# Optimization experiments

Measured on AMD Instinct MI355X. Metric: run time of the kernel, lower is better.

Reference implementation:

```python
import jax, jax.numpy as jnp
import numpy as np

D_P, D_T, D_F = 128, 256, 384
D = D_P + D_T + D_F            # 768
NUM_PART, NUM_TIMES, NUM_F0 = 64, 601, 360
NHEAD, NLAYERS, DFF = 12, 6, 2048
CTX, PRED = 1024, 64
BATCH = 8
NEG = -1e9


def sin_emb(vals, d, L, base=10000.0):
    # vectorized version of the per-scalar sin_embedding loop
    i = jnp.arange(d // 2, dtype=jnp.float32)
    wk = base ** (-i / d) * (d / L)
    ang = vals[..., None].astype(jnp.float32) * wk           # [..., d/2]
    return jnp.stack([jnp.sin(ang), jnp.cos(ang)], axis=-1).reshape(vals.shape + (d,))


def layernorm(x, g, b, eps=1e-5):
    mu = jnp.mean(x, axis=-1, keepdims=True)
    var = jnp.var(x, axis=-1, keepdims=True)
    return (x - mu) * jax.lax.rsqrt(var + eps) * g + b


def setup_inputs() -> dict:
    key = jax.random.key(0)
    ks = jax.random.split(key, 20)
    inp = {}
    inp['context_participant'] = jax.random.randint(ks[0], (BATCH, CTX), 0, NUM_PART)
    inp['context_time'] = jax.random.uniform(ks[1], (BATCH, CTX), jnp.float32) * 60.0
    inp['context_f0'] = jax.random.randint(ks[2], (BATCH, CTX), 0, NUM_F0)
    # learned / frozen tables
    inp['part_table'] = jax.random.normal(ks[3], (NUM_PART, D_P), jnp.float32)
    inp['time_table'] = sin_emb(jnp.arange(NUM_TIMES, dtype=jnp.float32), D_T, NUM_TIMES)
    inp['f0_table'] = sin_emb(jnp.arange(NUM_F0, dtype=jnp.float32), D_F, NUM_F0)
    inp['pad'] = jax.random.normal(ks[4], (D,), jnp.float32)
    s = 0.02
    inp['Wqkv'] = jax.random.normal(ks[5], (NLAYERS, 3 * D, D), jnp.float32) * s
    inp['bqkv'] = jnp.zeros((NLAYERS, 3 * D), jnp.float32)
    inp['Wo'] = jax.random.normal(ks[6], (NLAYERS, D, D), jnp.float32) * s
    inp['bo'] = jnp.zeros((NLAYERS, D), jnp.float32)
    inp['ln1_g'] = jnp.ones((NLAYERS, D), jnp.float32)
    inp['ln1_b'] = jnp.zeros((NLAYERS, D), jnp.float32)
    inp['W1'] = jax.random.normal(ks[7], (NLAYERS, DFF, D), jnp.float32) * s
    inp['b1'] = jnp.zeros((NLAYERS, DFF), jnp.float32)
    inp['W2'] = jax.random.normal(ks[8], (NLAYERS, D, DFF), jnp.float32) * s
    inp['b2'] = jnp.zeros((NLAYERS, D), jnp.float32)
    inp['ln2_g'] = jnp.ones((NLAYERS, D), jnp.float32)
    inp['ln2_b'] = jnp.zeros((NLAYERS, D), jnp.float32)
    return inp


def reference(context_participant, context_time, context_f0, part_table, time_table,
              f0_table, pad, Wqkv, bqkv, Wo, bo, ln1_g, ln1_b, W1, b1, W2, b2,
              ln2_g, ln2_b):
    B = context_participant.shape[0]
    emb = jnp.concatenate([
        part_table[context_participant],
        sin_emb(context_time, D_T, NUM_TIMES),
        f0_table[context_f0],
    ], axis=-1)                                               # [B, CTX, D]
    dummy = jnp.broadcast_to(pad[None, None, :], (B, PRED, D))
    x = jnp.concatenate([emb, dummy], axis=1)                 # [B, S, D]
    S = CTX + PRED
    # causal mask with -1e9 above diagonal; target block fully masked (incl. diag)
    mask = jnp.where(jnp.triu(jnp.ones((S, S), bool), k=1), NEG, 0.0).astype(jnp.float32)
    mask = mask.at[CTX:, CTX:].set(NEG)
    hd = D // NHEAD
    scale = 1.0 / jnp.sqrt(jnp.float32(hd))
    for l in range(NLAYERS):
        qkv = x @ Wqkv[l].T + bqkv[l]
        q, k, v = jnp.split(qkv, 3, axis=-1)
        q = q.reshape(B, S, NHEAD, hd)
        k = k.reshape(B, S, NHEAD, hd)
        v = v.reshape(B, S, NHEAD, hd)
        scores = jnp.einsum('bqhd,bkhd->bhqk', q, k) * scale + mask
        attn = jax.nn.softmax(scores, axis=-1)
        ctx = jnp.einsum('bhqk,bkhd->bqhd', attn, v).reshape(B, S, D)
        x = layernorm(x + (ctx @ Wo[l].T + bo[l]), ln1_g[l], ln1_b[l])
        ff = jax.nn.relu(x @ W1[l].T + b1[l]) @ W2[l].T + b2[l]
        x = layernorm(x + ff, ln2_g[l], ln2_b[l])
    pred = x[:, CTX:, :]
    pred_cat_logits = pred[:, :, :D_P] @ part_table.T
    pred_time_logits = pred[:, :, D_P:D_P + D_T] @ time_table.T
    pred_f0_logits = pred[:, :, D_P + D_T:] @ f0_table.T
    return (pred_cat_logits, pred_time_logits, pred_f0_logits)
```

## Files before the change

kernel.cpp:

```cpp
#include <hip/hip_runtime.h>
#include <hip/hip_bf16.h>
#include <math.h>

#define D_P 128
#define D_T 256
#define D_F 384
#define DIM 768
#define NUM_TIMES 601
#define NUM_F0 360
#define NHEAD 12
#define HD 64
#define NLAYERS 6
#define DFF 2048
#define CTX 1024
#define SEQ 1088
#define BATCH 8
#define ROWS (BATCH*SEQ)
#define TDIM3 (3*DIM)
#define PREDROWS 512

typedef unsigned short ushort_t;
typedef __attribute__((ext_vector_type(8))) short bfrag;
typedef __attribute__((ext_vector_type(4))) float f32x4;

__global__ void SequenceModel_30425548325019_kernel(unsigned short* out, int n, unsigned short v) {
  int i = blockIdx.x * 256 + threadIdx.x;
  if (i < n) out[i] = v;
}

__device__ inline short f2bf(float f) {
  unsigned u = __float_as_uint(f);
  unsigned r = (u + 0x7FFFu + ((u >> 16) & 1u)) >> 16;
  return (short)r;
}

__device__ inline void gload16(const void* g, void* l) {
  __builtin_amdgcn_global_load_lds(
      (const __attribute__((address_space(1))) unsigned*)g,
      (__attribute__((address_space(3))) unsigned*)l, 16, 0, 0);
}

__global__ __launch_bounds__(256) void cvt_bf16(const float* __restrict__ src,
                                                ushort_t* __restrict__ dst, int n) {
  int i = (blockIdx.x * 256 + threadIdx.x) * 4;
  if (i >= n) return;
  float4 v = *(const float4*)(src + i);
  dst[i + 0] = (ushort_t)f2bf(v.x);
  dst[i + 1] = (ushort_t)f2bf(v.y);
  dst[i + 2] = (ushort_t)f2bf(v.z);
  dst[i + 3] = (ushort_t)f2bf(v.w);
}

__global__ __launch_bounds__(256) void embed_kernel(
    const int* __restrict__ cp, const float* __restrict__ ct,
    const int* __restrict__ cf, const float* __restrict__ part,
    const float* __restrict__ f0t, const float* __restrict__ pad,
    float* __restrict__ x, ushort_t* __restrict__ xb) {
  int idx = blockIdx.x * 256 + threadIdx.x;
  if (idx >= ROWS * DIM) return;
  int d = idx % DIM;
  int row = idx / DIM;
  int b = row / SEQ, s = row - b * SEQ;
  float v;
  if (s >= CTX) {
    v = pad[d];
  } else if (d < D_P) {
    v = part[cp[b * CTX + s] * D_P + d];
  } else if (d < D_P + D_T) {
    int j = d - D_P;
    int i2 = j >> 1;
    float wk = powf(10000.f, -(float)i2 / (float)D_T) * ((float)D_T / (float)NUM_TIMES);
    float ang = ct[b * CTX + s] * wk;
    v = (j & 1) ? cosf(ang) : sinf(ang);
  } else {
    v = f0t[cf[b * CTX + s] * D_F + (d - D_P - D_T)];
  }
  x[idx] = v;
  xb[idx] = (ushort_t)f2bf(v);
}

#define BM 128
#define BN 128
#define BK 32

__global__ __launch_bounds__(256) void gemm_bb(
    const ushort_t* __restrict__ A, const ushort_t* __restrict__ B,
    const float* __restrict__ bias, const float* __restrict__ resid,
    float* __restrict__ C, ushort_t* __restrict__ Cb,
    int M, int N, int K, int relu, int qscale) {
  __shared__ short As[4 * BM * 8];
  __shared__ short Bs[4 * BN * 8];
  const int tid = threadIdx.x;
  const int wave = tid >> 6, lane = tid & 63;
  const int wr = wave >> 1, wc = wave & 1;
  const int l15 = lane & 15, l4 = lane >> 4;
  const int m0 = blockIdx.y * BM, n0 = blockIdx.x * BN;
  f32x4 acc[4][4] = {};

  for (int k0 = 0; k0 < K; k0 += BK) {
    __syncthreads();
    #pragma unroll
    for (int i = 0; i < 2; ++i) {
      int u = i * 256 + wave * 64 + lane;
      int row = u & 127, kg = u >> 7;
      gload16(A + (size_t)(m0 + row) * K + k0 + kg * 8, &As[(i * 256 + wave * 64) * 8]);
      gload16(B + (size_t)(n0 + row) * K + k0 + kg * 8, &Bs[(i * 256 + wave * 64) * 8]);
    }
    __syncthreads();
    bfrag a[4], b[4];
    #pragma unroll
    for (int f = 0; f < 4; ++f) {
      a[f] = *(const bfrag*)&As[(l4 * BM + wr * 64 + f * 16 + l15) * 8];
      b[f] = *(const bfrag*)&Bs[(l4 * BN + wc * 64 + f * 16 + l15) * 8];
    }
    #pragma unroll
    for (int i = 0; i < 4; ++i)
      #pragma unroll
      for (int j = 0; j < 4; ++j)
        acc[i][j] = __builtin_amdgcn_mfma_f32_16x16x32_bf16(a[i], b[j], acc[i][j], 0, 0, 0);
  }
  #pragma unroll
  for (int i = 0; i < 4; ++i) {
    int mbase = m0 + wr * 64 + i * 16 + l4 * 4;
    #pragma unroll
    for (int j = 0; j < 4; ++j) {
      int n = n0 + wc * 64 + j * 16 + l15;
      float bv = bias[n];
      #pragma unroll
      for (int r = 0; r < 4; ++r) {
        int m = mbase + r;
        float v = acc[i][j][r] + bv;
        if (resid) v += resid[(size_t)m * N + n];
        if (relu) v = fmaxf(v, 0.f);
        if (qscale && n < DIM) v *= 0.125f;
        if (C) C[(size_t)m * N + n] = v;
        if (Cb) Cb[(size_t)m * N + n] = (ushort_t)f2bf(v);
      }
    }
  }
}

__global__ __launch_bounds__(256) void gather_pred(const ushort_t* __restrict__ xb,
                                                   ushort_t* __restrict__ xpb) {
  int idx = blockIdx.x * 256 + threadIdx.x;
  if (idx >= PREDROWS * DIM) return;
  int r = idx / DIM, d = idx - r * DIM;
  int b = r >> 6, rr = r & 63;
  xpb[idx] = xb[(size_t)(b * SEQ + CTX + rr) * DIM + d];
}

__global__ __launch_bounds__(256) void head_mfma(
    const ushort_t* __restrict__ A, const ushort_t* __restrict__ B,
    float* __restrict__ C, int N, int K, int lda, int coloff) {
  __shared__ short As[4 * BM * 8];
  __shared__ short Bs[4 * BN * 8];
  const int tid = threadIdx.x;
  const int wave = tid >> 6, lane = tid & 63;
  const int wr = wave >> 1, wc = wave & 1;
  const int l15 = lane & 15, l4 = lane >> 4;
  const int m0 = blockIdx.y * BM, n0 = blockIdx.x * BN;
  f32x4 acc[4][4] = {};

  for (int k0 = 0; k0 < K; k0 += BK) {
    __syncthreads();
    #pragma unroll
    for (int i = 0; i < 2; ++i) {
      int u = i * 256 + wave * 64 + lane;
      int row = u & 127, kg = u >> 7;
      gload16(A + (size_t)(m0 + row) * lda + coloff + k0 + kg * 8,
              &As[(i * 256 + wave * 64) * 8]);
      gload16(B + (size_t)(n0 + row) * K + k0 + kg * 8,
              &Bs[(i * 256 + wave * 64) * 8]);
    }
    __syncthreads();
    bfrag a[4], b[4];
    #pragma unroll
    for (int f = 0; f < 4; ++f) {
      a[f] = *(const bfrag*)&As[(l4 * BM + wr * 64 + f * 16 + l15) * 8];
      b[f] = *(const bfrag*)&Bs[(l4 * BN + wc * 64 + f * 16 + l15) * 8];
    }
    #pragma unroll
    for (int i = 0; i < 4; ++i)
      #pragma unroll
      for (int j = 0; j < 4; ++j)
        acc[i][j] = __builtin_amdgcn_mfma_f32_16x16x32_bf16(a[i], b[j], acc[i][j], 0, 0, 0);
  }
  #pragma unroll
  for (int i = 0; i < 4; ++i) {
    int mbase = m0 + wr * 64 + i * 16 + l4 * 4;
    #pragma unroll
    for (int j = 0; j < 4; ++j) {
      int n = n0 + wc * 64 + j * 16 + l15;
      if (n >= N) continue;
      #pragma unroll
      for (int r = 0; r < 4; ++r)
        C[(size_t)(mbase + r) * N + n] = acc[i][j][r];
    }
  }
}

#define QBLK 64
__global__ __launch_bounds__(256) void attn_mfma(const ushort_t* __restrict__ qkv,
                                                 ushort_t* __restrict__ outb) {
  const int qt = blockIdx.x, h = blockIdx.y, b = blockIdx.z;
  const int q0 = qt * QBLK;
  __shared__ short Qs[8 * 64 * 8];
  __shared__ short Ks[8 * 32 * 8];
  __shared__ short Vt[4 * 64 * 9];
  __shared__ short Ps[4 * 64 * 9];
  __shared__ float SO[64 * 68];
  __shared__ float alphaS[64], linvS[64];
  const int tid = threadIdx.x;
  const int wave = tid >> 6, lane = tid & 63;
  const int l15 = lane & 15, l4 = lane >> 4;
  const int srow = tid >> 3, skg = tid & 7;
  const int smrow = tid >> 2, smc = tid & 3;
  const int qf = wave;

  #pragma unroll
  for (int i = 0; i < 2; ++i) {
    int s = tid + 256 * i;
    int r = s >> 3, kg = s & 7;
    const ushort_t* qp = qkv + (size_t)(b * SEQ + q0 + r) * TDIM3 + h * HD + kg * 8;
    *(bfrag*)&Qs[(kg * 64 + ((r + kg) & 63)) * 8] = *(const bfrag*)qp;
  }
  float mrun = -1e30f, lrun = 0.f;
  f32x4 o[4] = {};
  const int nkt = (q0 < CTX) ? (q0 + QBLK) / 32 : (CTX / 32);

  for (int kt = 0; kt < nkt; ++kt) {
    const int k0 = kt * 32;
    __syncthreads();
    {
      const ushort_t* kp = qkv + (size_t)(b * SEQ + k0 + srow) * TDIM3 + DIM + h * HD + skg * 8;
      *(bfrag*)&Ks[(skg * 32 + ((srow + skg) & 31)) * 8] = *(const bfrag*)kp;
      bfrag vv = *(const bfrag*)(kp + DIM);
      int kg2 = srow >> 3, j = srow & 7, db = skg * 8;
      #pragma unroll
      for (int e = 0; e < 8; ++e)
        Vt[(kg2 * 64 + db + e) * 9 + j] = vv[e];
    }
    __syncthreads();
    #pragma unroll
    for (int jk = 0; jk < 2; ++jk) {
      f32x4 s = {};
      #pragma unroll
      for (int t = 0; t < 2; ++t) {
        int kg = t * 4 + l4;
        int ar = qf * 16 + l15;
        bfrag a = *(const bfrag*)&Qs[(kg * 64 + ((ar + kg) & 63)) * 8];
        int br = jk * 16 + l15;
        bfrag bb = *(const bfrag*)&Ks[(kg * 32 + ((br + kg) & 31)) * 8];
        s = __builtin_amdgcn_mfma_f32_16x16x32_bf16(a, bb, s, 0, 0, 0);
      }
      #pragma unroll
      for (int r = 0; r < 4; ++r)
        SO[(qf * 16 + l4 * 4 + r) * 33 + jk * 16 + l15] = s[r];
    }
    __syncthreads();
    {
      const int qglob = q0 + smrow;
      float p[8];
      float tm = -1e30f;
      #pragma unroll
      for (int i = 0; i < 8; ++i) {
        int kg = k0 + smc * 8 + i;
        float s = SO[smrow * 33 + smc * 8 + i];
        bool allowed = (qglob < CTX) ? (kg <= qglob) : true;
        p[i] = allowed ? s : -1e30f;
        tm = fmaxf(tm, p[i]);
      }
      tm = fmaxf(tm, __shfl_xor(tm, 1));
      tm = fmaxf(tm, __shfl_xor(tm, 2));
      float mn = fmaxf(mrun, tm);
      float alpha = __expf(mrun - mn);
      float ls = 0.f;
      #pragma unroll
      for (int i = 0; i < 8; ++i) { p[i] = __expf(p[i] - mn); ls += p[i]; }
      ls += __shfl_xor(ls, 1);
      ls += __shfl_xor(ls, 2);
      lrun = lrun * alpha + ls;
      mrun = mn;
      if (smc == 0) alphaS[smrow] = alpha;
      short* pd = &Ps[(smc * 64 + smrow) * 9];
      #pragma unroll
      for (int i = 0; i < 8; ++i) pd[i] = f2bf(p[i]);
    }
    __syncthreads();
    {
      #pragma unroll
      for (int r = 0; r < 4; ++r) {
        float ar = alphaS[qf * 16 + l4 * 4 + r];
        #pragma unroll
        for (int df = 0; df < 4; ++df) o[df][r] *= ar;
      }
      bfrag pa = *(const bfrag*)&Ps[(l4 * 64 + qf * 16 + l15) * 9];
      #pragma unroll
      for (int df = 0; df < 4; ++df) {
        bfrag v = *(const bfrag*)&Vt[(l4 * 64 + df * 16 + l15) * 9];
        o[df] = __builtin_amdgcn_mfma_f32_16x16x32_bf16(pa, v, o[df], 0, 0, 0);
      }
    }
  }
  if (smc == 0) linvS[smrow] = 1.f / lrun;
  __syncthreads();
  #pragma unroll
  for (int r = 0; r < 4; ++r) {
    float li = linvS[qf * 16 + l4 * 4 + r];
    #pragma unroll
    for (int df = 0; df < 4; ++df)
      SO[(qf * 16 + l4 * 4 + r) * 68 + df * 16 + l15] = o[df][r] * li;
  }
  __syncthreads();
  #pragma unroll
  for (int i = 0; i < 2; ++i) {
    int s = tid + 256 * i;
    int r = s >> 3, kg = s & 7;
    ushort_t* dst = outb + (size_t)(b * SEQ + q0 + r) * DIM + h * HD + kg * 8;
    const float* sp = &SO[r * 68 + kg * 8];
    bfrag t;
    #pragma unroll
    for (int e = 0; e < 8; ++e) t[e] = f2bf(sp[e]);
    *(bfrag*)dst = t;
  }
}

__global__ __launch_bounds__(256) void ln_kernel(float* __restrict__ x,
                                                 const float* __restrict__ g,
                                                 const float* __restrict__ bb,
                                                 ushort_t* __restrict__ xb) {
  const int row = blockIdx.x;
  float* p = x + (size_t)row * DIM;
  ushort_t* pb = xb + (size_t)row * DIM;
  const int tid = threadIdx.x;
  float v0 = p[tid], v1 = p[tid + 256], v2 = p[tid + 512];
  float s1 = v0 + v1 + v2;
  float s2 = v0 * v0 + v1 * v1 + v2 * v2;
  #pragma unroll
  for (int off = 32; off >= 1; off >>= 1) {
    s1 += __shfl_down(s1, off);
    s2 += __shfl_down(s2, off);
  }
  __shared__ float r1[4], r2[4];
  int wid = tid >> 6;
  if ((tid & 63) == 0) { r1[wid] = s1; r2[wid] = s2; }
  __syncthreads();
  s1 = r1[0] + r1[1] + r1[2] + r1[3];
  s2 = r2[0] + r2[1] + r2[2] + r2[3];
  const float mu = s1 * (1.f / DIM);
  const float var = s2 * (1.f / DIM) - mu * mu;
  const float rs = rsqrtf(var + 1e-5f);
  float o0 = (v0 - mu) * rs * g[tid]       + bb[tid];
  float o1 = (v1 - mu) * rs * g[tid + 256] + bb[tid + 256];
  float o2 = (v2 - mu) * rs * g[tid + 512] + bb[tid + 512];
  p[tid] = o0;       pb[tid] = (ushort_t)f2bf(o0);
  p[tid + 256] = o1; pb[tid + 256] = (ushort_t)f2bf(o1);
  p[tid + 512] = o2; pb[tid + 512] = (ushort_t)f2bf(o2);
}

extern "C" void kernel_launch(void* const* d_in, const int* in_sizes, int n_in,
                              void* d_out, int out_size, void* d_ws, size_t ws_size,
                              hipStream_t stream) {
  const size_t N_X    = (size_t)ROWS * DIM;
  const size_t N_XB   = N_X / 2;
  const size_t N_BUFB = (size_t)ROWS * TDIM3 / 2;
  const size_t N_CTB  = N_X / 2;
  const size_t N_WQ   = 10616832 / 2;
  const size_t N_WO   = 3538944 / 2;
  const size_t N_W1   = 9437184 / 2;
  const size_t N_W2   = 9437184 / 2;
  const size_t N_PT   = 8192 / 2;
  const size_t N_TT   = 153856 / 2;
  const size_t N_FT   = 138240 / 2;
  const size_t N_XPB  = (size_t)PREDROWS * DIM / 2;
  size_t need = (N_X + N_XB + N_BUFB + N_CTB + N_WQ + N_WO + N_W1 + N_W2 +
                 N_PT + N_TT + N_FT + N_XPB) * sizeof(float);
  if (ws_size < need) {
    SequenceModel_30425548325019_kernel<<<(out_size + 255) / 256, 256, 0, stream>>>(
        (unsigned short*)d_out, out_size, (unsigned short)0x4280);
    return;
  }

  const int*   cp    = (const int*)d_in[0];
  const float* ct    = (const float*)d_in[1];
  const int*   cf    = (const int*)d_in[2];
  const float* part  = (const float*)d_in[3];
  const float* timet = (const float*)d_in[4];
  const float* f0t   = (const float*)d_in[5];
  const float* pad   = (const float*)d_in[6];
  const float* Wqkv  = (const float*)d_in[7];
  const float* bqkv  = (const float*)d_in[8];
  const float* Wo    = (const float*)d_in[9];
  const float* bo    = (const float*)d_in[10];
  const float* ln1g  = (const float*)d_in[11];
  const float* ln1b  = (const float*)d_in[12];
  const float* W1    = (const float*)d_in[13];
  const float* b1    = (const float*)d_in[14];
  const float* W2    = (const float*)d_in[15];
  const float* b2    = (const float*)d_in[16];
  const float* ln2g  = (const float*)d_in[17];
  const float* ln2b  = (const float*)d_in[18];

  float* base = (float*)d_ws;
  float*    x      = base;                 base += N_X;
  ushort_t* xb     = (ushort_t*)base;      base += N_XB;
  ushort_t* bufb   = (ushort_t*)base;      base += N_BUFB;
  ushort_t* ctxbb  = (ushort_t*)base;      base += N_CTB;
  ushort_t* Wqkvb  = (ushort_t*)base;      base += N_WQ;
  ushort_t* Wob    = (ushort_t*)base;      base += N_WO;
  ushort_t* W1b    = (ushort_t*)base;      base += N_W1;
  ushort_t* W2b    = (ushort_t*)base;      base += N_W2;
  ushort_t* partb  = (ushort_t*)base;      base += N_PT;
  ushort_t* timetb = (ushort_t*)base;      base += N_TT;
  ushort_t* f0tb   = (ushort_t*)base;      base += N_FT;
  ushort_t* xpb    = (ushort_t*)base;

  cvt_bf16<<<(10616832 / 4 + 255) / 256, 256, 0, stream>>>(Wqkv, Wqkvb, 10616832);
  cvt_bf16<<<(3538944 / 4 + 255) / 256, 256, 0, stream>>>(Wo, Wob, 3538944);
  cvt_bf16<<<(9437184 / 4 + 255) / 256, 256, 0, stream>>>(W1, W1b, 9437184);
  cvt_bf16<<<(9437184 / 4 + 255) / 256, 256, 0, stream>>>(W2, W2b, 9437184);
  cvt_bf16<<<(8192 / 4 + 255) / 256, 256, 0, stream>>>(part, partb, 8192);
  cvt_bf16<<<(153856 / 4 + 255) / 256, 256, 0, stream>>>(timet, timetb, 153856);
  cvt_bf16<<<(138240 / 4 + 255) / 256, 256, 0, stream>>>(f0t, f0tb, 138240);

  embed_kernel<<<(ROWS * DIM + 255) / 256, 256, 0, stream>>>(cp, ct, cf, part, f0t, pad, x, xb);

  for (int l = 0; l < NLAYERS; ++l) {
    gemm_bb<<<dim3(TDIM3 / BN, ROWS / BM), 256, 0, stream>>>(
        xb, Wqkvb + (size_t)l * TDIM3 * DIM, bqkv + l * TDIM3, nullptr,
        nullptr, bufb, ROWS, TDIM3, DIM, 0, 1);
    attn_mfma<<<dim3(SEQ / QBLK, NHEAD, BATCH), 256, 0, stream>>>(bufb, ctxbb);
    gemm_bb<<<dim3(DIM / BN, ROWS / BM), 256, 0, stream>>>(
        ctxbb, Wob + (size_t)l * DIM * DIM, bo + l * DIM, x,
        x, nullptr, ROWS, DIM, DIM, 0, 0);
    ln_kernel<<<ROWS, 256, 0, stream>>>(x, ln1g + l * DIM, ln1b + l * DIM, xb);
    gemm_bb<<<dim3(DFF / BN, ROWS / BM), 256, 0, stream>>>(
        xb, W1b + (size_t)l * DFF * DIM, b1 + l * DFF, nullptr,
        nullptr, bufb, ROWS, DFF, DIM, 1, 0);
    gemm_bb<<<dim3(DIM / BN, ROWS / BM), 256, 0, stream>>>(
        bufb, W2b + (size_t)l * DIM * DFF, b2 + l * DIM, x,
        x, nullptr, ROWS, DIM, DFF, 0, 0);
    ln_kernel<<<ROWS, 256, 0, stream>>>(x, ln2g + l * DIM, ln2b + l * DIM, xb);
  }

  float* out = (float*)d_out;
  gather_pred<<<(PREDROWS * DIM + 255) / 256, 256, 0, stream>>>(xb, xpb);
  head_mfma<<<dim3(1, PREDROWS / BM), 256, 0, stream>>>(xpb, partb, out, 64, 128, DIM, 0);
  head_mfma<<<dim3(5, PREDROWS / BM), 256, 0, stream>>>(xpb, timetb, out + 32768, NUM_TIMES, 256, DIM, 128);
  head_mfma<<<dim3(3, PREDROWS / BM), 256, 0, stream>>>(xpb, f0tb, out + 32768 + 307712, NUM_F0, 384, DIM, 384);
}
```

Measured before the change: 3.038 ms.

## Hold Q in registers, load K directly from global, widen key tile to 64

The attention kernel now keeps its Q fragments in registers and reads K fragments straight from global memory into MFMA operands, so the Q and K shared-memory staging is gone. The key block grows from 32 to 64, which halves the number of loop iterations and the barriers they carry, and one barrier per iteration is dropped. The risk is that K is now read from global memory by every wave without reuse through LDS, and the output staging now uses a stride of 65 that may be misaligned for the vectorized reads.

New measurement: 3.069 ms. No clear change (+1.0%).

```diff
diff --git a/kernel.cpp b/kernel.cpp
--- a/kernel.cpp
+++ b/kernel.cpp
@@ -200,72 +200,63 @@
 }
 
 #define QBLK 64
+#define KBLK 64
 __global__ __launch_bounds__(256) void attn_mfma(const ushort_t* __restrict__ qkv,
                                                  ushort_t* __restrict__ outb) {
   const int qt = blockIdx.x, h = blockIdx.y, b = blockIdx.z;
   const int q0 = qt * QBLK;
-  __shared__ short Qs[8 * 64 * 8];
-  __shared__ short Ks[8 * 32 * 8];
-  __shared__ short Vt[4 * 64 * 9];
-  __shared__ short Ps[4 * 64 * 9];
-  __shared__ float SO[64 * 68];
+  __shared__ short Vt[8 * 64 * 9];
+  __shared__ short Ps[8 * 64 * 9];
+  __shared__ float SO[64 * 65];
   __shared__ float alphaS[64], linvS[64];
   const int tid = threadIdx.x;
   const int wave = tid >> 6, lane = tid & 63;
   const int l15 = lane & 15, l4 = lane >> 4;
-  const int srow = tid >> 3, skg = tid & 7;
   const int smrow = tid >> 2, smc = tid & 3;
   const int qf = wave;
 
-  #pragma unroll
-  for (int i = 0; i < 2; ++i) {
-    int s = tid + 256 * i;
-    int r = s >> 3, kg = s & 7;
-    const ushort_t* qp = qkv + (size_t)(b * SEQ + q0 + r) * TDIM3 + h * HD + kg * 8;
-    *(bfrag*)&Qs[(kg * 64 + ((r + kg) & 63)) * 8] = *(const bfrag*)qp;
-  }
+  const size_t qrow_addr = (size_t)(b * SEQ + q0 + qf * 16 + l15) * TDIM3 + h * HD;
+  bfrag aq0 = *(const bfrag*)(qkv + qrow_addr + 0 * 32 + l4 * 8);
+  bfrag aq1 = *(const bfrag*)(qkv + qrow_addr + 1 * 32 + l4 * 8);
+
   float mrun = -1e30f, lrun = 0.f;
   f32x4 o[4] = {};
-  const int nkt = (q0 < CTX) ? (q0 + QBLK) / 32 : (CTX / 32);
+  const int nkt = (q0 < CTX) ? (q0 + QBLK) / KBLK : (CTX / KBLK);
 
   for (int kt = 0; kt < nkt; ++kt) {
-    const int k0 = kt * 32;
-    __syncthreads();
-    {
-      const ushort_t* kp = qkv + (size_t)(b * SEQ + k0 + srow) * TDIM3 + DIM + h * HD + skg * 8;
-      *(bfrag*)&Ks[(skg * 32 + ((srow + skg) & 31)) * 8] = *(const bfrag*)kp;
-      bfrag vv = *(const bfrag*)(kp + DIM);
-      int kg2 = srow >> 3, j = srow & 7, db = skg * 8;
+    const int k0 = kt * KBLK;
+    __syncthreads();
+    #pragma unroll
+    for (int i = 0; i < 2; ++i) {
+      int u = tid + 256 * i;
+      int krow = u >> 3, dg = u & 7;
+      bfrag vv = *(const bfrag*)(qkv + (size_t)(b * SEQ + k0 + krow) * TDIM3 + 2 * DIM + h * HD + dg * 8);
+      int kg = krow >> 3, j = krow & 7;
       #pragma unroll
       for (int e = 0; e < 8; ++e)
-        Vt[(kg2 * 64 + db + e) * 9 + j] = vv[e];
-    }
-    __syncthreads();
-    #pragma unroll
-    for (int jk = 0; jk < 2; ++jk) {
+        Vt[(kg * 64 + dg * 8 + e) * 9 + j] = vv[e];
+    }
+    #pragma unroll
+    for (int jk = 0; jk < 4; ++jk) {
+      const size_t krow_addr = (size_t)(b * SEQ + k0 + jk * 16 + l15) * TDIM3 + DIM + h * HD;
+      bfrag bk0 = *(const bfrag*)(qkv + krow_addr + 0 * 32 + l4 * 8);
+      bfrag bk1 = *(const bfrag*)(qkv + krow_addr + 1 * 32 + l4 * 8);
       f32x4 s = {};
-      #pragma unroll
-      for (int t = 0; t < 2; ++t) {
-        int kg = t * 4 + l4;
-        int ar = qf * 16 + l15;
-        bfrag a = *(const bfrag*)&Qs[(kg * 64 + ((ar + kg) & 63)) * 8];
-        int br = jk * 16 + l15;
-        bfrag bb = *(const bfrag*)&Ks[(kg * 32 + ((br + kg) & 31)) * 8];
-        s = __builtin_amdgcn_mfma_f32_16x16x32_bf16(a, bb, s, 0, 0, 0);
-      }
+      s = __builtin_amdgcn_mfma_f32_16x16x32_bf16(aq0, bk0, s, 0, 0, 0);
+      s = __builtin_amdgcn_mfma_f32_16x16x32_bf16(aq1, bk1, s, 0, 0, 0);
       #pragma unroll
       for (int r = 0; r < 4; ++r)
-        SO[(qf * 16 + l4 * 4 + r) * 33 + jk * 16 + l15] = s[r];
+        SO[(qf * 16 + l4 * 4 + r) * 65 + jk * 16 + l15] = s[r];
     }
     __syncthreads();
     {
       const int qglob = q0 + smrow;
-      float p[8];
+      float p[16];
       float tm = -1e30f;
       #pragma unroll
-      for (int i = 0; i < 8; ++i) {
-        int kg = k0 + smc * 8 + i;
-        float s = SO[smrow * 33 + smc * 8 + i];
+      for (int i = 0; i < 16; ++i) {
+        int kg = k0 + smc * 16 + i;
+        float s = SO[smrow * 65 + smc * 16 + i];
         bool allowed = (qglob < CTX) ? (kg <= qglob) : true;
         p[i] = allowed ? s : -1e30f;
         tm = fmaxf(tm, p[i]);
@@ -276,15 +267,16 @@
       float alpha = __expf(mrun - mn);
       float ls = 0.f;
       #pragma unroll
-      for (int i = 0; i < 8; ++i) { p[i] = __expf(p[i] - mn); ls += p[i]; }
+      for (int i = 0; i < 16; ++i) { p[i] = __expf(p[i] - mn); ls += p[i]; }
       ls += __shfl_xor(ls, 1);
       ls += __shfl_xor(ls, 2);
       lrun = lrun * alpha + ls;
       mrun = mn;
       if (smc == 0) alphaS[smrow] = alpha;
-      short* pd = &Ps[(smc * 64 + smrow) * 9];
-      #pragma unroll
-      for (int i = 0; i < 8; ++i) pd[i] = f2bf(p[i]);
+      short* pd0 = &Ps[((smc * 2 + 0) * 64 + smrow) * 9];
+      short* pd1 = &Ps[((smc * 2 + 1) * 64 + smrow) * 9];
+      #pragma unroll
+      for (int i = 0; i < 8; ++i) { pd0[i] = f2bf(p[i]); pd1[i] = f2bf(p[i + 8]); }
     }
     __syncthreads();
     {
@@ -294,11 +286,14 @@
         #pragma unroll
         for (int df = 0; df < 4; ++df) o[df][r] *= ar;
       }
-      bfrag pa = *(const bfrag*)&Ps[(l4 * 64 + qf * 16 + l15) * 9];
-      #pragma unroll
-      for (int df = 0; df < 4; ++df) {
-        bfrag v = *(const bfrag*)&Vt[(l4 * 64 + df * 16 + l15) * 9];
-        o[df] = __builtin_amdgcn_mfma_f32_16x16x32_bf16(pa, v, o[df], 0, 0, 0);
+      #pragma unroll
+      for (int c = 0; c < 2; ++c) {
+        bfrag pa = *(const bfrag*)&Ps[((c * 4 + l4) * 64 + qf * 16 + l15) * 9];
+        #pragma unroll
+        for (int df = 0; df < 4; ++df) {
+          bfrag v = *(const bfrag*)&Vt[((c * 4 + l4) * 64 + df * 16 + l15) * 9];
+          o[df] = __builtin_amdgcn_mfma_f32_16x16x32_bf16(pa, v, o[df], 0, 0, 0);
+        }
       }
     }
   }
@@ -309,7 +304,7 @@
     float li = linvS[qf * 16 + l4 * 4 + r];
     #pragma unroll
     for (int df = 0; df < 4; ++df)
-      SO[(qf * 16 + l4 * 4 + r) * 68 + df * 16 + l15] = o[df][r] * li;
+      SO[(qf * 16 + l4 * 4 + r) * 65 + df * 16 + l15] = o[df][r] * li;
   }
   __syncthreads();
   #pragma unroll
@@ -317,7 +312,7 @@
     int s = tid + 256 * i;
     int r = s >> 3, kg = s & 7;
     ushort_t* dst = outb + (size_t)(b * SEQ + q0 + r) * DIM + h * HD + kg * 8;
-    const float* sp = &SO[r * 68 + kg * 8];
+    const float* sp = &SO[r * 65 + kg * 8];
     bfrag t;
     #pragma unroll
     for (int e = 0; e < 8; ++e) t[e] = f2bf(sp[e]);
```
